# Performance work log

Hardware: AMD Instinct MI355X
Metric: run time of the kernel (lower is better)

The kernel has to match this reference:

```python
import jax, jax.numpy as jnp
import numpy as np

B, C, IMG, P = 16, 3, 224, 16
HP = IMG // P          # 14
NP = HP * HP           # 196 patches
PD = C * P * P         # 768 patch_dim
DIM, OUT = 768, 1024
DI, NS, DC, DTR = 2 * DIM, 16, 4, 48  # mamba: d_inner, d_state, d_conv, dt_rank
NL = 2


def _ln(x, g, b, eps=1e-5):
    m = x.mean(-1, keepdims=True)
    v = ((x - m) ** 2).mean(-1, keepdims=True)
    return (x - m) / jnp.sqrt(v + eps) * g + b


def _gelu(x):
    return jax.nn.gelu(x, approximate=False)


def _mamba_block(x, in_w, in_b, conv_w, conv_b, xproj_w, dt_w, dt_b, Alog, D, out_w, out_b):
    # x: [B, L, DIM]
    Bb, L, _ = x.shape
    xr = x @ in_w + in_b                      # [B, L, 2*DI]
    xi, res = jnp.split(xr, 2, axis=-1)
    # causal depthwise conv1d over L
    xp = jnp.pad(xi, ((0, 0), (DC - 1, 0), (0, 0)))
    xc = conv_b + sum(xp[:, k:k + L, :] * conv_w[:, k] for k in range(DC))
    xi = jax.nn.silu(xc)
    dbc = xi @ xproj_w                        # [B, L, DTR + 2*NS]
    delta = jax.nn.softplus(dbc[..., :DTR] @ dt_w + dt_b)   # [B, L, DI]
    Bm = dbc[..., DTR:DTR + NS]               # [B, L, NS]
    Cm = dbc[..., DTR + NS:]                  # [B, L, NS]
    A = -jnp.exp(Alog)                        # [DI, NS]
    dA = jnp.exp(delta[..., None] * A)                       # [B, L, DI, NS]
    dBu = delta[..., None] * Bm[:, :, None, :] * xi[..., None]

    def step(h, inp):
        dA_t, dBu_t, C_t = inp
        h = dA_t * h + dBu_t                  # [B, DI, NS]
        y = jnp.einsum('bdn,bn->bd', h, C_t)
        return h, y

    h0 = jnp.zeros((Bb, DI, NS), x.dtype)
    _, ys = jax.lax.scan(step, h0, (dA.transpose(1, 0, 2, 3),
                                    dBu.transpose(1, 0, 2, 3),
                                    Cm.transpose(1, 0, 2)))
    y = ys.transpose(1, 0, 2) + D * xi        # [B, L, DI]
    y = y * jax.nn.silu(res)
    return y @ out_w + out_b


def setup_inputs() -> dict:
    key = jax.random.key(0)
    ks = iter(jax.random.split(key, 40))

    def rn(shape, s=0.02):
        return jax.random.normal(next(ks), shape, jnp.float32) * s

    inp = {
        'img': jax.random.normal(next(ks), (B, C, IMG, IMG), jnp.float32),
        'sa_w': rn((1, 2, 7, 7), 0.1),
        'pe_w': rn((PD, DIM)), 'pe_b': jnp.zeros((DIM,), jnp.float32),
        'pos_emb': rn((1, NP, DIM), 1.0),
        'm_in_w': rn((NL, DIM, 2 * DI)), 'm_in_b': jnp.zeros((NL, 2 * DI), jnp.float32),
        'm_conv_w': rn((NL, DI, DC), 0.1), 'm_conv_b': jnp.zeros((NL, DI), jnp.float32),
        'm_xproj_w': rn((NL, DI, DTR + 2 * NS)),
        'm_dt_w': rn((NL, DTR, DI)), 'm_dt_b': rn((NL, DI), 0.01),
        'm_Alog': jnp.tile(jnp.log(jnp.arange(1, NS + 1, dtype=jnp.float32))[None, None, :], (NL, DI, 1)),
        'm_D': jnp.ones((NL, DI), jnp.float32),
        'm_out_w': rn((NL, DI, DIM)), 'm_out_b': jnp.zeros((NL, DIM), jnp.float32),
        'em_w': rn((DIM, OUT)), 'em_b': jnp.zeros((OUT,), jnp.float32),
        'em_g': jnp.ones((OUT,), jnp.float32), 'em_bt': jnp.zeros((OUT,), jnp.float32),
        'att_w': rn((OUT, OUT)), 'att_b': jnp.zeros((OUT,), jnp.float32),
        'att_g': jnp.ones((OUT,), jnp.float32), 'att_bt': jnp.zeros((OUT,), jnp.float32),
        'lat_g': jnp.ones((OUT,), jnp.float32), 'lat_bt': jnp.zeros((OUT,), jnp.float32),
    }
    return inp


def reference(img, sa_w, pe_w, pe_b, pos_emb,
              m_in_w, m_in_b, m_conv_w, m_conv_b, m_xproj_w,
              m_dt_w, m_dt_b, m_Alog, m_D, m_out_w, m_out_b,
              em_w, em_b, em_g, em_bt, att_w, att_b, att_g, att_bt,
              lat_g, lat_bt):
    # spatial attention gate
    avg = img.mean(axis=1, keepdims=True)
    mx = img.max(axis=1, keepdims=True)
    a = jnp.concatenate([avg, mx], axis=1)                    # [B,2,H,W]
    a = jax.lax.conv_general_dilated(a, sa_w, (1, 1), [(3, 3), (3, 3)],
                                     dimension_numbers=('NCHW', 'OIHW', 'NCHW'))
    img = img * jax.nn.sigmoid(a)
    # patchify: b c (h p1)(w p2) -> b (h w) (p1 p2 c)
    x = img.reshape(B, C, HP, P, HP, P).transpose(0, 2, 4, 3, 5, 1).reshape(B, NP, PD)
    x = x @ pe_w + pe_b                                       # [B, NP, DIM]
    x = x + pos_emb[:, :NP]
    for i in range(NL):
        x = _mamba_block(x, m_in_w[i], m_in_b[i], m_conv_w[i], m_conv_b[i],
                         m_xproj_w[i], m_dt_w[i], m_dt_b[i], m_Alog[i], m_D[i],
                         m_out_w[i], m_out_b[i])
    y = _gelu(_ln(x @ em_w + em_b, em_g, em_bt))              # [B, NP, OUT]
    z = jax.nn.softmax(_gelu(_ln(y @ att_w + att_b, att_g, att_bt)), axis=1)
    pooled = (y * z).sum(axis=1)                              # [B, OUT]
    return _ln(pooled, lat_g, lat_bt)
```

## Files before the change

### kernel.cpp

```cpp
#include <hip/hip_runtime.h>
#include <math.h>

static constexpr int NB = 16;
static constexpr int NC = 3;
static constexpr int IM = 224;
static constexpr int IMP = IM * IM;
static constexpr int HPq = 14;
static constexpr int NPq = 196;
static constexpr int OUTq = 1024;
static constexpr int DIq = 1536;
static constexpr int ROWS = NB * NPq;
static constexpr int MPAD = 3200;

typedef __bf16 bf8_t __attribute__((ext_vector_type(8)));
typedef float f4_t __attribute__((ext_vector_type(4)));
typedef const __attribute__((address_space(1))) unsigned int cgu32;
typedef __attribute__((address_space(3))) unsigned int lu32;

__device__ inline unsigned short f2bf(float x) {
    unsigned u = __builtin_bit_cast(unsigned, x);
    unsigned r = (u + 0x7FFFu + ((u >> 16) & 1u)) >> 16;
    return (unsigned short)r;
}
__device__ inline float bf2f(unsigned short v) {
    return __builtin_bit_cast(float, (unsigned)v << 16);
}
__device__ inline float fast_sig(float x) {
    return __builtin_amdgcn_rcpf(1.f + __expf(-x));
}

template<int CTRL>
__device__ inline float dpp_add(float x) {
    int v = __builtin_amdgcn_update_dpp(0, __builtin_bit_cast(int, x), CTRL, 0xF, 0xF, true);
    return x + __builtin_bit_cast(float, v);
}

__global__ __launch_bounds__(256) void k_avgmax(const float* __restrict__ img, float* __restrict__ am) {
    int idx = blockIdx.x * 256 + threadIdx.x;
    if (idx >= NB * IMP / 4) return;
    int p4 = (idx % (IMP / 4)) * 4, b = idx / (IMP / 4);
    const float* ib = img + (size_t)b * NC * IMP + p4;
    float4 c0 = *(const float4*)ib;
    float4 c1 = *(const float4*)(ib + IMP);
    float4 c2 = *(const float4*)(ib + 2 * IMP);
    float4 av, mx;
    av.x = (c0.x + c1.x + c2.x) * (1.f / 3.f); mx.x = fmaxf(c0.x, fmaxf(c1.x, c2.x));
    av.y = (c0.y + c1.y + c2.y) * (1.f / 3.f); mx.y = fmaxf(c0.y, fmaxf(c1.y, c2.y));
    av.z = (c0.z + c1.z + c2.z) * (1.f / 3.f); mx.z = fmaxf(c0.z, fmaxf(c1.z, c2.z));
    av.w = (c0.w + c1.w + c2.w) * (1.f / 3.f); mx.w = fmaxf(c0.w, fmaxf(c1.w, c2.w));
    *(float4*)(am + (size_t)(b * 2 + 0) * IMP + p4) = av;
    *(float4*)(am + (size_t)(b * 2 + 1) * IMP + p4) = mx;
}

__global__ __launch_bounds__(256) void k_gatepatch(const float* __restrict__ img, const float* __restrict__ am,
                                                   const float* __restrict__ saw, unsigned short* __restrict__ G) {
    int quad = blockIdx.x * 256 + threadIdx.x;
    if (quad >= NB * IMP / 4) return;
    int pq = quad % (IMP / 4), b = quad / (IMP / 4);
    int x0 = (pq % 56) * 4;
    int y = pq / 56;
    float acc0 = 0.f, acc1 = 0.f, acc2 = 0.f, acc3 = 0.f;
    const bool lok = (x0 >= 4), rok = (x0 <= IM - 8);
    #pragma unroll
    for (int ci = 0; ci < 2; ci++) {
        const float* amc = am + (size_t)(b * 2 + ci) * IMP;
        const float* wc = saw + ci * 49;
        #pragma unroll
        for (int kh = 0; kh < 7; kh++) {
            int yy = y + kh - 3;
            if (yy < 0 || yy >= IM) continue;
            const float* rowp = amc + yy * IM;
            float4 lv = lok ? *(const float4*)(rowp + x0 - 4) : make_float4(0.f, 0.f, 0.f, 0.f);
            float4 mv = *(const float4*)(rowp + x0);
            float4 rv = rok ? *(const float4*)(rowp + x0 + 4) : make_float4(0.f, 0.f, 0.f, 0.f);
            float f[12] = {lv.x, lv.y, lv.z, lv.w, mv.x, mv.y, mv.z, mv.w, rv.x, rv.y, rv.z, rv.w};
            #pragma unroll
            for (int kw = 0; kw < 7; kw++) {
                float w = wc[kh * 7 + kw];
                acc0 = fmaf(w, f[kw + 1], acc0);
                acc1 = fmaf(w, f[kw + 2], acc1);
                acc2 = fmaf(w, f[kw + 3], acc2);
                acc3 = fmaf(w, f[kw + 4], acc3);
            }
        }
    }
    float s0 = fast_sig(acc0), s1 = fast_sig(acc1), s2 = fast_sig(acc2), s3 = fast_sig(acc3);
    const float* ib = img + (size_t)b * NC * IMP + y * IM + x0;
    float4 c0 = *(const float4*)ib;
    float4 c1 = *(const float4*)(ib + IMP);
    float4 c2 = *(const float4*)(ib + 2 * IMP);
    int hy = y >> 4, py = y & 15, hx = x0 >> 4, px0 = x0 & 15;
    size_t base = ((size_t)(b * NPq + hy * HPq + hx) * 768) + (size_t)(py * 16 + px0) * 3;
    ushort4 o0, o1, o2;
    o0.x = f2bf(c0.x * s0); o0.y = f2bf(c1.x * s0); o0.z = f2bf(c2.x * s0);
    o0.w = f2bf(c0.y * s1);
    o1.x = f2bf(c1.y * s1); o1.y = f2bf(c2.y * s1);
    o1.z = f2bf(c0.z * s2); o1.w = f2bf(c1.z * s2);
    o2.x = f2bf(c2.z * s2);
    o2.y = f2bf(c0.w * s3); o2.z = f2bf(c1.w * s3); o2.w = f2bf(c2.w * s3);
    *(ushort4*)(G + base + 0) = o0;
    *(ushort4*)(G + base + 4) = o1;
    *(ushort4*)(G + base + 8) = o2;
}

__global__ __launch_bounds__(256) void k_transpose_bf(const float* __restrict__ W, unsigned short* __restrict__ Wt,
                                                      int K, int N) {
    __shared__ float t[32][33];
    int n0 = blockIdx.x * 32, k0 = blockIdx.y * 32;
    int c = threadIdx.x & 31, r8 = threadIdx.x >> 5;
    #pragma unroll
    for (int i = 0; i < 4; i++) {
        int r = r8 + i * 8;
        t[r][c] = W[(size_t)(k0 + r) * N + n0 + c];
    }
    __syncthreads();
    #pragma unroll
    for (int i = 0; i < 4; i++) {
        int r = r8 + i * 8;
        Wt[(size_t)(n0 + r) * K + k0 + c] = f2bf(t[c][r]);
    }
}

enum { EPI_NONE = 0, EPI_POSEMB = 1, EPI_SPLIT = 2 };

template<int EPI, bool CBF>
__global__ __launch_bounds__(256) void k_gemm_bf(const unsigned short* __restrict__ A,
                                                 const unsigned short* __restrict__ Wt,
                                                 const float* __restrict__ bias,
                                                 void* __restrict__ Cv, int ldc,
                                                 int M, int N, int K,
                                                 const float* __restrict__ extra,
                                                 float* __restrict__ C2) {
    constexpr int BM = 128, BN = 64;
    __shared__ __align__(16) unsigned short As[2][BM * 64];
    __shared__ __align__(16) unsigned short Bs[2][BN * 64];
    const int bm = blockIdx.y * BM, bn = blockIdx.x * BN;
    const int tid = threadIdx.x;
    const int lane = tid & 63;
    const int wbase = tid & ~63;
    const int wr = ((tid >> 7) & 1) * 64;
    const int wc = ((tid >> 6) & 1) * 32;
    const int lr = lane & 15, lq = lane >> 4;

    f4_t acc[4][2] = {};

    auto stage = [&](int buf, int k0) {
        #pragma unroll
        for (int i = 0; i < 4; i++) {
            int gid2 = i * 256 + tid;
            int r = gid2 >> 3, g = gid2 & 7;
            const unsigned short* src = A + (size_t)(bm + r) * K + k0 + ((g ^ (r & 7)) * 8);
            __builtin_amdgcn_global_load_lds((cgu32*)src,
                (lu32*)&As[buf][(i * 256 + wbase) * 8], 16, 0, 0);
        }
        #pragma unroll
        for (int i = 0; i < 2; i++) {
            int gid2 = i * 256 + tid;
            int r = gid2 >> 3, g = gid2 & 7;
            const unsigned short* src = Wt + (size_t)(bn + r) * K + k0 + ((g ^ (r & 7)) * 8);
            __builtin_amdgcn_global_load_lds((cgu32*)src,
                (lu32*)&Bs[buf][(i * 256 + wbase) * 8], 16, 0, 0);
        }
    };

    stage(0, 0);
    __syncthreads();
    int cur = 0;
    for (int k0 = 0; k0 < K; k0 += 64) {
        if (k0 + 64 < K) stage(cur ^ 1, k0 + 64);
        #pragma unroll
        for (int h = 0; h < 2; h++) {
            bf8_t af[4], bfr[2];
            #pragma unroll
            for (int mb = 0; mb < 4; mb++) {
                int row = wr + mb * 16 + lr;
                int g = h * 4 + lq;
                af[mb] = *(const bf8_t*)&As[cur][row * 64 + ((g ^ (row & 7)) * 8)];
            }
            #pragma unroll
            for (int nb = 0; nb < 2; nb++) {
                int rn = wc + nb * 16 + lr;
                int g = h * 4 + lq;
                bfr[nb] = *(const bf8_t*)&Bs[cur][rn * 64 + ((g ^ (rn & 7)) * 8)];
            }
            #pragma unroll
            for (int mb = 0; mb < 4; mb++)
                #pragma unroll
                for (int nb = 0; nb < 2; nb++)
                    acc[mb][nb] = __builtin_amdgcn_mfma_f32_16x16x32_bf16(af[mb], bfr[nb], acc[mb][nb], 0, 0, 0);
        }
        __syncthreads();
        cur ^= 1;
    }

    #pragma unroll
    for (int mb = 0; mb < 4; mb++) {
        #pragma unroll
        for (int nb = 0; nb < 2; nb++) {
            int col = bn + wc + nb * 16 + lr;
            #pragma unroll
            for (int q = 0; q < 4; q++) {
                int row = bm + wr + mb * 16 + lq * 4 + q;
                if (row < M) {
                    float v = acc[mb][nb][q];
                    if (bias) v += bias[col];
                    if (EPI == EPI_SPLIT) {
                        if (col < DIq) ((unsigned short*)Cv)[(size_t)row * DIq + col] = f2bf(v);
                        else           C2[(size_t)row * DIq + (col - DIq)] = v * fast_sig(v);
                    } else {
                        if (EPI == EPI_POSEMB) v += extra[(size_t)(row % NPq) * N + col];
                        if (CBF) ((unsigned short*)Cv)[(size_t)row * ldc + col] = f2bf(v);
                        else     ((float*)Cv)[(size_t)row * ldc + col] = v;
                    }
                }
            }
        }
    }
}

static constexpr int XP_KS = 4;
static constexpr int XP_KC = 1536 / XP_KS;

__global__ __launch_bounds__(256) void k_xproj_part(const float* __restrict__ xi2, const float* __restrict__ W,
                                                    float* __restrict__ part) {
    __shared__ float As[32][65];
    __shared__ __align__(16) float Bs[64][80];
    int m0 = blockIdx.x * 32;
    int kc0 = blockIdx.y * XP_KC;
    int tid = threadIdx.x;
    int row = tid >> 3, cg = (tid & 7) * 10;
    float acc[10] = {};
    for (int k0 = 0; k0 < XP_KC; k0 += 64) {
        #pragma unroll
        for (int i = 0; i < 2; i++) {
            int id = tid + i * 256;
            int r = id >> 4, c4 = (id & 15) * 4;
            float4 v = *(const float4*)(xi2 + (size_t)(m0 + r) * 1536 + kc0 + k0 + c4);
            As[r][c4] = v.x; As[r][c4 + 1] = v.y; As[r][c4 + 2] = v.z; As[r][c4 + 3] = v.w;
        }
        #pragma unroll
        for (int i = 0; i < 5; i++) {
            int id = tid + i * 256;
            int r = id / 20, c4 = (id % 20) * 4;
            *(float4*)&Bs[r][c4] = *(const float4*)(W + (size_t)(kc0 + k0 + r) * 80 + c4);
        }
        __syncthreads();
        #pragma unroll
        for (int kk = 0; kk < 64; kk++) {
            float a = As[row][kk];
            #pragma unroll
            for (int j = 0; j < 10; j++)
                acc[j] = fmaf(a, Bs[kk][cg + j], acc[j]);
        }
        __syncthreads();
    }
    float* p = part + ((size_t)blockIdx.y * ROWS + m0 + row) * 80 + cg;
    #pragma unroll
    for (int j = 0; j < 10; j++) p[j] = acc[j];
}

static constexpr int DT_RPB = 4;
__global__ __launch_bounds__(384) void k_dtred(const float* __restrict__ part, const float* __restrict__ W,
                                               const float* __restrict__ bias, float* __restrict__ de,
                                               float* __restrict__ dbc) {
    int r0 = blockIdx.x * DT_RPB;
    int tid = threadIdx.x;
    __shared__ float ds[DT_RPB][80];
    if (tid < DT_RPB * 80) {
        int row = tid / 80, col = tid % 80;
        const int S = ROWS * 80;
        const float* p = part + (size_t)(r0 + row) * 80 + col;
        float s = p[0] + p[S] + p[2 * S] + p[3 * S];
        ds[row][col] = s;
        if (col >= 48) dbc[(size_t)(r0 + row) * 80 + col] = s;
    }
    __syncthreads();
    int j = tid * 4;
    float4 b = *(const float4*)(bias + j);
    float4 a0 = b, a1 = b, a2 = b, a3 = b;
    for (int k = 0; k < 48; k++) {
        float4 w = *(const float4*)(W + (size_t)k * 1536 + j);
        float d0 = ds[0][k], d1 = ds[1][k], d2 = ds[2][k], d3 = ds[3][k];
        a0.x = fmaf(d0, w.x, a0.x); a0.y = fmaf(d0, w.y, a0.y); a0.z = fmaf(d0, w.z, a0.z); a0.w = fmaf(d0, w.w, a0.w);
        a1.x = fmaf(d1, w.x, a1.x); a1.y = fmaf(d1, w.y, a1.y); a1.z = fmaf(d1, w.z, a1.z); a1.w = fmaf(d1, w.w, a1.w);
        a2.x = fmaf(d2, w.x, a2.x); a2.y = fmaf(d2, w.y, a2.y); a2.z = fmaf(d2, w.z, a2.z); a2.w = fmaf(d2, w.w, a2.w);
        a3.x = fmaf(d3, w.x, a3.x); a3.y = fmaf(d3, w.y, a3.y); a3.z = fmaf(d3, w.z, a3.z); a3.w = fmaf(d3, w.w, a3.w);
    }
    auto sp = [](float v) { return (v > 20.f) ? v : log1pf(expf(v)); };
    float4 o;
    o.x = sp(a0.x); o.y = sp(a0.y); o.z = sp(a0.z); o.w = sp(a0.w);
    *(float4*)(de + (size_t)(r0 + 0) * 1536 + j) = o;
    o.x = sp(a1.x); o.y = sp(a1.y); o.z = sp(a1.z); o.w = sp(a1.w);
    *(float4*)(de + (size_t)(r0 + 1) * 1536 + j) = o;
    o.x = sp(a2.x); o.y = sp(a2.y); o.z = sp(a2.z); o.w = sp(a2.w);
    *(float4*)(de + (size_t)(r0 + 2) * 1536 + j) = o;
    o.x = sp(a3.x); o.y = sp(a3.y); o.z = sp(a3.z); o.w = sp(a3.w);
    *(float4*)(de + (size_t)(r0 + 3) * 1536 + j) = o;
}

__global__ __launch_bounds__(256) void k_conv_silu(const unsigned short* __restrict__ xr2, const float* __restrict__ cw,
                                                   const float* __restrict__ cb, float* __restrict__ xi2) {
    int idx4 = blockIdx.x * 256 + threadIdx.x;
    if (idx4 >= ROWS * DIq / 4) return;
    int d4 = (idx4 % (DIq / 4)) * 4;
    int bt = idx4 / (DIq / 4);
    int t = bt % NPq, b = bt / NPq;
    const unsigned short* base = xr2 + (size_t)b * NPq * DIq + d4;
    float4 s = *(const float4*)(cb + d4);
    float4 w0 = *(const float4*)(cw + (d4 + 0) * 4);
    float4 w1 = *(const float4*)(cw + (d4 + 1) * 4);
    float4 w2 = *(const float4*)(cw + (d4 + 2) * 4);
    float4 w3 = *(const float4*)(cw + (d4 + 3) * 4);
    if (t >= 3) {
        ushort4 v = *(const ushort4*)(base + (size_t)(t - 3) * DIq);
        s.x = fmaf(bf2f(v.x), w0.x, s.x); s.y = fmaf(bf2f(v.y), w1.x, s.y);
        s.z = fmaf(bf2f(v.z), w2.x, s.z); s.w = fmaf(bf2f(v.w), w3.x, s.w);
    }
    if (t >= 2) {
        ushort4 v = *(const ushort4*)(base + (size_t)(t - 2) * DIq);
        s.x = fmaf(bf2f(v.x), w0.y, s.x); s.y = fmaf(bf2f(v.y), w1.y, s.y);
        s.z = fmaf(bf2f(v.z), w2.y, s.z); s.w = fmaf(bf2f(v.w), w3.y, s.w);
    }
    if (t >= 1) {
        ushort4 v = *(const ushort4*)(base + (size_t)(t - 1) * DIq);
        s.x = fmaf(bf2f(v.x), w0.z, s.x); s.y = fmaf(bf2f(v.y), w1.z, s.y);
        s.z = fmaf(bf2f(v.z), w2.z, s.z); s.w = fmaf(bf2f(v.w), w3.z, s.w);
    }
    {
        ushort4 v = *(const ushort4*)(base + (size_t)t * DIq);
        s.x = fmaf(bf2f(v.x), w0.w, s.x); s.y = fmaf(bf2f(v.y), w1.w, s.y);
        s.z = fmaf(bf2f(v.z), w2.w, s.z); s.w = fmaf(bf2f(v.w), w3.w, s.w);
    }
    float4 xo;
    xo.x = s.x * fast_sig(s.x); xo.y = s.y * fast_sig(s.y);
    xo.z = s.z * fast_sig(s.z); xo.w = s.w * fast_sig(s.w);
    *(float4*)(xi2 + (size_t)bt * DIq + d4) = xo;
}

static constexpr int STB = 28;

__global__ __launch_bounds__(256) void k_scan(const float* __restrict__ delta, const float* __restrict__ xi2,
                                              const float* __restrict__ dbc, const float* __restrict__ sres,
                                              const float* __restrict__ Alog, const float* __restrict__ Dv,
                                              unsigned short* __restrict__ ys) {
    const int b = blockIdx.x;
    const int d0 = blockIdx.y * 32;
    const int tid = threadIdx.x;
    const int dl = tid >> 3;
    const int np = tid & 7;
    const int d = d0 + dl;
    const float A0 = -__expf(Alog[d * 16 + np]);
    const float A1 = -__expf(Alog[d * 16 + np + 8]);
    const float Dd = Dv[d];
    const int tr = tid >> 5;
    const int dls = tid & 31;

    __shared__ float4 sdu[2][STB][32];
    __shared__ float sbc[2][STB][32];

    const float* gde = delta + ((size_t)b * NPq + tr) * DIq + d0 + dls;
    const float* gu  = xi2   + ((size_t)b * NPq + tr) * DIq + d0 + dls;
    const float* gsr = sres  + ((size_t)b * NPq + tr) * DIq + d0 + dls;
    const float* gbc = dbc   + ((size_t)b * NPq + tr) * 80 + 48 + dls;
    unsigned short* gy = ys + (size_t)b * NPq * DIq + d;

    float rde[4], ru[4], rsr[4], rbc[4];

    auto stageLoad = [&](int c) {
        const int t0 = c * STB;
        #pragma unroll
        for (int j = 0; j < 3; j++) {
            int off = (t0 + 8 * j) * DIq;
            rde[j] = gde[off];
            ru[j]  = gu[off];
            rsr[j] = gsr[off];
            rbc[j] = gbc[(t0 + 8 * j) * 80];
        }
        if (tid < 128) {
            int off = (t0 + 24) * DIq;
            rde[3] = gde[off];
            ru[3]  = gu[off];
            rsr[3] = gsr[off];
            rbc[3] = gbc[(t0 + 24) * 80];
        }
    };
    auto stageWrite = [&](int buf) {
        const int pi = (dls & 7) * 4 + (dls >> 3);
        #pragma unroll
        for (int j = 0; j < 3; j++) {
            int t = tr + 8 * j;
            sdu[buf][t][dls] = make_float4(rde[j], ru[j], rsr[j], 0.f);
            sbc[buf][t][pi] = rbc[j];
        }
        if (tid < 128) {
            int t = tr + 24;
            sdu[buf][t][dls] = make_float4(rde[3], ru[3], rsr[3], 0.f);
            sbc[buf][t][pi] = rbc[3];
        }
    };

    stageLoad(0);
    stageWrite(0);
    __syncthreads();

    float h0 = 0.f, h1 = 0.f;
    int cur = 0;
    for (int c = 0; c < 7; c++) {
        if (c < 6) stageLoad(c + 1);
        #pragma unroll 4
        for (int t = 0; t < STB; t++) {
            float4 du = sdu[cur][t][dl];
            float4 bc = *(const float4*)&sbc[cur][t][np * 4];
            float a0 = __expf(du.x * A0), a1 = __expf(du.x * A1);
            float deu = du.x * du.y;
            h0 = fmaf(a0, h0, deu * bc.x);
            h1 = fmaf(a1, h1, deu * bc.y);
            float p = fmaf(h1, bc.w, h0 * bc.z);
            p = dpp_add<0xB1>(p);
            p = dpp_add<0x4E>(p);
            p = dpp_add<0x141>(p);
            if (np == 0) gy[(size_t)(c * STB + t) * DIq] = f2bf(fmaf(Dd, du.y, p) * du.z);
        }
        if (c < 6) stageWrite(cur ^ 1);
        __syncthreads();
        cur ^= 1;
    }
}

template<bool OBF>
__global__ __launch_bounds__(256) void k_ln_gelu(const float* __restrict__ in, const float* __restrict__ g,
                                                 const float* __restrict__ bt, void* __restrict__ outv) {
    int row = blockIdx.x;
    const float* x = in + (size_t)row * OUTq;
    float4 v = ((const float4*)x)[threadIdx.x];
    float s = v.x + v.y + v.z + v.w;
    float ss = v.x * v.x + v.y * v.y + v.z * v.z + v.w * v.w;
    #pragma unroll
    for (int off = 32; off >= 1; off >>= 1) { s += __shfl_down(s, off); ss += __shfl_down(ss, off); }
    __shared__ float sh[10];
    int wid = threadIdx.x >> 6, lid = threadIdx.x & 63;
    if (lid == 0) { sh[wid] = s; sh[4 + wid] = ss; }
    __syncthreads();
    if (threadIdx.x == 0) {
        float S = sh[0] + sh[1] + sh[2] + sh[3], SS = sh[4] + sh[5] + sh[6] + sh[7];
        float m = S * (1.f / OUTq);
        float var = SS * (1.f / OUTq) - m * m;
        sh[8] = m; sh[9] = rsqrtf(var + 1e-5f);
    }
    __syncthreads();
    float m = sh[8], rst = sh[9];
    float4 gv = ((const float4*)g)[threadIdx.x];
    float4 bv = ((const float4*)bt)[threadIdx.x];
    float4 o;
    float y0 = (v.x - m) * rst * gv.x + bv.x; o.x = 0.5f * y0 * (1.f + erff(y0 * 0.70710678118f));
    float y1 = (v.y - m) * rst * gv.y + bv.y; o.y = 0.5f * y1 * (1.f + erff(y1 * 0.70710678118f));
    float y2 = (v.z - m) * rst * gv.z + bv.z; o.z = 0.5f * y2 * (1.f + erff(y2 * 0.70710678118f));
    float y3 = (v.w - m) * rst * gv.w + bv.w; o.w = 0.5f * y3 * (1.f + erff(y3 * 0.70710678118f));
    if (OBF) {
        ushort4 o4;
        o4.x = f2bf(o.x); o4.y = f2bf(o.y); o4.z = f2bf(o.z); o4.w = f2bf(o.w);
        ((ushort4*)((unsigned short*)outv + (size_t)row * OUTq))[threadIdx.x] = o4;
    } else {
        ((float4*)((float*)outv + (size_t)row * OUTq))[threadIdx.x] = o;
    }
}

__global__ __launch_bounds__(256) void k_softpool(const float* __restrict__ gm, const unsigned short* __restrict__ ym,
                                                  float* __restrict__ pooled) {
    int b = blockIdx.y;
    int jl = threadIdx.x & 63;
    int j = blockIdx.x * 64 + jl;
    int tc = threadIdx.x >> 6;
    const float* gb = gm + (size_t)b * NPq * OUTq + j;
    const unsigned short* yb = ym + (size_t)b * NPq * OUTq + j;
    int t0 = tc * 49;
    float m = -1e30f, s = 0.f, ps = 0.f;
    for (int t = t0; t < t0 + 49; t++) {
        float g = gb[(size_t)t * OUTq];
        float y = bf2f(yb[(size_t)t * OUTq]);
        float mn = fmaxf(m, g);
        float sc = __expf(m - mn);
        float e = __expf(g - mn);
        s = fmaf(s, sc, e);
        ps = fmaf(ps, sc, y * e);
        m = mn;
    }
    __shared__ float sm[4][64], ssum[4][64], sps[4][64];
    sm[tc][jl] = m; ssum[tc][jl] = s; sps[tc][jl] = ps;
    __syncthreads();
    if (tc == 0) {
        float m0 = sm[0][jl], m1 = sm[1][jl], m2 = sm[2][jl], m3 = sm[3][jl];
        float mt = fmaxf(fmaxf(m0, m1), fmaxf(m2, m3));
        float e0 = __expf(m0 - mt), e1 = __expf(m1 - mt);
        float e2 = __expf(m2 - mt), e3 = __expf(m3 - mt);
        float st = ssum[0][jl] * e0 + ssum[1][jl] * e1 + ssum[2][jl] * e2 + ssum[3][jl] * e3;
        float pt = sps[0][jl] * e0 + sps[1][jl] * e1 + sps[2][jl] * e2 + sps[3][jl] * e3;
        pooled[b * OUTq + j] = pt / st;
    }
}

__global__ __launch_bounds__(256) void k_final_ln(const float* __restrict__ p, const float* __restrict__ g,
                                                  const float* __restrict__ bt, float* __restrict__ out) {
    int row = blockIdx.x;
    const float* x = p + (size_t)row * OUTq;
    float4 v = ((const float4*)x)[threadIdx.x];
    float s = v.x + v.y + v.z + v.w;
    float ss = v.x * v.x + v.y * v.y + v.z * v.z + v.w * v.w;
    #pragma unroll
    for (int off = 32; off >= 1; off >>= 1) { s += __shfl_down(s, off); ss += __shfl_down(ss, off); }
    __shared__ float sh[10];
    int wid = threadIdx.x >> 6, lid = threadIdx.x & 63;
    if (lid == 0) { sh[wid] = s; sh[4 + wid] = ss; }
    __syncthreads();
    if (threadIdx.x == 0) {
        float S = sh[0] + sh[1] + sh[2] + sh[3], SS = sh[4] + sh[5] + sh[6] + sh[7];
        float m = S * (1.f / OUTq);
        float var = SS * (1.f / OUTq) - m * m;
        sh[8] = m; sh[9] = rsqrtf(var + 1e-5f);
    }
    __syncthreads();
    float m = sh[8], rst = sh[9];
    float4 gv = ((const float4*)g)[threadIdx.x];
    float4 bv = ((const float4*)bt)[threadIdx.x];
    float4 o;
    o.x = (v.x - m) * rst * gv.x + bv.x;
    o.y = (v.y - m) * rst * gv.y + bv.y;
    o.z = (v.z - m) * rst * gv.z + bv.z;
    o.w = (v.w - m) * rst * gv.w + bv.w;
    ((float4*)(out + (size_t)row * OUTq))[threadIdx.x] = o;
}

extern "C" void kernel_launch(void* const* d_in, const int* in_sizes, int n_in,
                              void* d_out, int out_size, void* d_ws, size_t ws_size,
                              hipStream_t stream) {
    const float* img   = (const float*)d_in[0];
    const float* sa_w  = (const float*)d_in[1];
    const float* pe_w  = (const float*)d_in[2];
    const float* pe_b  = (const float*)d_in[3];
    const float* pos   = (const float*)d_in[4];
    const float* in_w  = (const float*)d_in[5];
    const float* in_b  = (const float*)d_in[6];
    const float* cv_w  = (const float*)d_in[7];
    const float* cv_b  = (const float*)d_in[8];
    const float* xp_w  = (const float*)d_in[9];
    const float* dt_w  = (const float*)d_in[10];
    const float* dt_b  = (const float*)d_in[11];
    const float* Alog  = (const float*)d_in[12];
    const float* Dv    = (const float*)d_in[13];
    const float* ot_w  = (const float*)d_in[14];
    const float* ot_b  = (const float*)d_in[15];
    const float* em_w  = (const float*)d_in[16];
    const float* em_b  = (const float*)d_in[17];
    const float* em_g  = (const float*)d_in[18];
    const float* em_bt = (const float*)d_in[19];
    const float* at_w  = (const float*)d_in[20];
    const float* at_b  = (const float*)d_in[21];
    const float* at_g  = (const float*)d_in[22];
    const float* at_bt = (const float*)d_in[23];
    const float* la_g  = (const float*)d_in[24];
    const float* la_bt = (const float*)d_in[25];

    char* ws = (char*)d_ws;
    auto al = [](size_t x) { return (x + 255) & ~(size_t)255; };
    size_t SZ_am   = (size_t)NB * 2 * IMP * 4;
    size_t SZ_G    = (size_t)MPAD * 768 * 2;
    size_t SZ_x    = (size_t)MPAD * 768 * 2;
    size_t SZ_xr2  = (size_t)ROWS * DIq * 2;
    size_t SZ_xi2  = (size_t)ROWS * DIq * 4;
    size_t SZ_de   = SZ_xi2;
    size_t SZ_dbc  = (size_t)ROWS * 80 * 4;
    size_t SZ_ys   = (size_t)MPAD * DIq * 2;
    size_t SZ_sres = SZ_xi2;
    size_t SZ_yem  = (size_t)MPAD * 1024 * 2;
    size_t SZ_pool = (size_t)NB * OUTq * 4;
    size_t SZ_part = (size_t)XP_KS * ROWS * 80 * 4;

    size_t o_am   = 0;
    size_t o_G    = al(o_am + SZ_am);
    size_t o_x    = al(o_G + SZ_G);
    size_t o_xr2  = al(o_x + SZ_x);
    size_t o_xi2  = al(o_xr2 + SZ_xr2);
    size_t o_de   = al(o_xi2 + SZ_xi2);
    size_t o_dbc  = al(o_de + SZ_de);
    size_t o_ys   = al(o_dbc + SZ_dbc);
    size_t o_sres = al(o_ys + SZ_ys);
    size_t o_yem  = al(o_sres + SZ_sres);
    size_t o_pool = al(o_yem + SZ_yem);
    size_t o_part = al(o_pool + SZ_pool);

    size_t o_wpe  = al(o_part + SZ_part);
    size_t o_win0 = al(o_wpe  + (size_t)768 * 768 * 2);
    size_t o_win1 = al(o_win0 + (size_t)3072 * 768 * 2);
    size_t o_wot0 = al(o_win1 + (size_t)3072 * 768 * 2);
    size_t o_wot1 = al(o_wot0 + (size_t)768 * 1536 * 2);
    size_t o_wem  = al(o_wot1 + (size_t)768 * 1536 * 2);
    size_t o_wat  = al(o_wem  + (size_t)1024 * 768 * 2);

    float* am    = (float*)(ws + o_am);
    unsigned short* G   = (unsigned short*)(ws + o_G);
    unsigned short* x   = (unsigned short*)(ws + o_x);
    unsigned short* xr2 = (unsigned short*)(ws + o_xr2);
    float* xi2   = (float*)(ws + o_xi2);
    float* de    = (float*)(ws + o_de);
    float* dbc   = (float*)(ws + o_dbc);
    unsigned short* ys = (unsigned short*)(ws + o_ys);
    float* sres  = (float*)(ws + o_sres);
    unsigned short* yem = (unsigned short*)(ws + o_yem);
    float* pool  = (float*)(ws + o_pool);
    float* part  = (float*)(ws + o_part);
    unsigned short* wpe  = (unsigned short*)(ws + o_wpe);
    unsigned short* win0 = (unsigned short*)(ws + o_win0);
    unsigned short* win1 = (unsigned short*)(ws + o_win1);
    unsigned short* wot0 = (unsigned short*)(ws + o_wot0);
    unsigned short* wot1 = (unsigned short*)(ws + o_wot1);
    unsigned short* wem  = (unsigned short*)(ws + o_wem);
    unsigned short* wat  = (unsigned short*)(ws + o_wat);
    float* t1  = (float*)(ws + o_de);
    float* t2  = (float*)(ws + o_xi2);
    float* gat = (float*)(ws + o_sres);

    k_transpose_bf<<<dim3(768 / 32, 768 / 32), 256, 0, stream>>>(pe_w, wpe, 768, 768);
    k_transpose_bf<<<dim3(3072 / 32, 768 / 32), 256, 0, stream>>>(in_w, win0, 768, 3072);
    k_transpose_bf<<<dim3(3072 / 32, 768 / 32), 256, 0, stream>>>(in_w + (size_t)768 * 3072, win1, 768, 3072);
    k_transpose_bf<<<dim3(768 / 32, 1536 / 32), 256, 0, stream>>>(ot_w, wot0, 1536, 768);
    k_transpose_bf<<<dim3(768 / 32, 1536 / 32), 256, 0, stream>>>(ot_w + (size_t)1536 * 768, wot1, 1536, 768);
    k_transpose_bf<<<dim3(1024 / 32, 768 / 32), 256, 0, stream>>>(em_w, wem, 768, 1024);
    k_transpose_bf<<<dim3(1024 / 32, 1024 / 32), 256, 0, stream>>>(at_w, wat, 1024, 1024);

    int nq = NB * IMP / 4;
    k_avgmax<<<(nq + 255) / 256, 256, 0, stream>>>(img, am);
    k_gatepatch<<<(nq + 255) / 256, 256, 0, stream>>>(img, am, sa_w, G);

    dim3 blk(256);
    k_gemm_bf<EPI_POSEMB, true><<<dim3(12, 25), blk, 0, stream>>>(G, wpe, pe_b, x, 768, ROWS, 768, 768,
                                                                  pos, nullptr);

    for (int l = 0; l < 2; l++) {
        const unsigned short* win = l ? win1 : win0;
        const unsigned short* wot = l ? wot1 : wot0;
        k_gemm_bf<EPI_SPLIT, true><<<dim3(48, 25), blk, 0, stream>>>(x, win, in_b + l * 3072, xr2, DIq,
                                                                     ROWS, 3072, 768, nullptr, sres);
        int nc4 = ROWS * DIq / 4;
        k_conv_silu<<<(nc4 + 255) / 256, 256, 0, stream>>>(xr2, cv_w + (size_t)l * DIq * 4, cv_b + l * DIq, xi2);
        k_xproj_part<<<dim3(ROWS / 32, XP_KS), blk, 0, stream>>>(xi2, xp_w + (size_t)l * 1536 * 80, part);
        k_dtred<<<ROWS / DT_RPB, 384, 0, stream>>>(part, dt_w + (size_t)l * 48 * 1536, dt_b + l * 1536, de, dbc);
        k_scan<<<dim3(16, 48), blk, 0, stream>>>(de, xi2, dbc, sres, Alog + (size_t)l * 1536 * 16,
                                                 Dv + l * 1536, ys);
        k_gemm_bf<EPI_NONE, true><<<dim3(12, 25), blk, 0, stream>>>(ys, wot, ot_b + l * 768, x, 768,
                                                                    ROWS, 768, 1536, nullptr, nullptr);
    }

    k_gemm_bf<EPI_NONE, false><<<dim3(16, 25), blk, 0, stream>>>(x, wem, em_b, t1, 1024, ROWS, 1024, 768,
                                                                 nullptr, nullptr);
    k_ln_gelu<true><<<ROWS, 256, 0, stream>>>(t1, em_g, em_bt, yem);
    k_gemm_bf<EPI_NONE, false><<<dim3(16, 25), blk, 0, stream>>>(yem, wat, at_b, t2, 1024, ROWS, 1024, 1024,
                                                                 nullptr, nullptr);
    k_ln_gelu<false><<<ROWS, 256, 0, stream>>>(t2, at_g, at_bt, gat);
    k_softpool<<<dim3(16, NB), 256, 0, stream>>>(gat, yem, pool);
    k_final_ln<<<NB, 256, 0, stream>>>(pool, la_g, la_bt, (float*)d_out);
}
```

Baseline: 503.7 us.

## Store mamba intermediates in bf16, merge transposes, add 128x128 in-proj GEMM

Moves xi2 (conv+silu output) and the silu(res) gate from fp32 to bf16 storage. The scan now packs both into one 32-bit word in shared memory, and the x-proj kernel reads bf16. The seven weight-transpose launches become a single kernel, and the in-projection uses a new 128x128-tile single-buffered GEMM. The intent is to cut memory traffic and launch overhead, at the cost of lower intermediate precision and no double buffering in the new GEMM.

```diff
diff --git a/kernel.cpp b/kernel.cpp
--- a/kernel.cpp
+++ b/kernel.cpp
@@ -14,6 +14,7 @@
 
 typedef __bf16 bf8_t __attribute__((ext_vector_type(8)));
 typedef float f4_t __attribute__((ext_vector_type(4)));
+typedef unsigned short us8 __attribute__((ext_vector_type(8)));
 typedef const __attribute__((address_space(1))) unsigned int cgu32;
 typedef __attribute__((address_space(3))) unsigned int lu32;
 
@@ -103,10 +104,23 @@
     *(ushort4*)(G + base + 8) = o2;
 }
 
-__global__ __launch_bounds__(256) void k_transpose_bf(const float* __restrict__ W, unsigned short* __restrict__ Wt,
-                                                      int K, int N) {
+__global__ __launch_bounds__(256) void k_transpose_all(const float* pe_w, const float* in_w, const float* ot_w,
+                                                       const float* em_w, const float* at_w,
+                                                       unsigned short* wpe, unsigned short* win0, unsigned short* win1,
+                                                       unsigned short* wot0, unsigned short* wot1,
+                                                       unsigned short* wem, unsigned short* wat) {
+    int bid = blockIdx.x;
+    const float* W; unsigned short* Wt; int K, N, local;
+    if (bid < 576)       { W = pe_w; Wt = wpe; K = 768; N = 768; local = bid; }
+    else if (bid < 2880) { W = in_w; Wt = win0; K = 768; N = 3072; local = bid - 576; }
+    else if (bid < 5184) { W = in_w + (size_t)768 * 3072; Wt = win1; K = 768; N = 3072; local = bid - 2880; }
+    else if (bid < 6336) { W = ot_w; Wt = wot0; K = 1536; N = 768; local = bid - 5184; }
+    else if (bid < 7488) { W = ot_w + (size_t)1536 * 768; Wt = wot1; K = 1536; N = 768; local = bid - 6336; }
+    else if (bid < 8256) { W = em_w; Wt = wem; K = 768; N = 1024; local = bid - 7488; }
+    else                 { W = at_w; Wt = wat; K = 1024; N = 1024; local = bid - 8256; }
+    int gx = N / 32;
+    int n0 = (local % gx) * 32, k0 = (local / gx) * 32;
     __shared__ float t[32][33];
-    int n0 = blockIdx.x * 32, k0 = blockIdx.y * 32;
     int c = threadIdx.x & 31, r8 = threadIdx.x >> 5;
     #pragma unroll
     for (int i = 0; i < 4; i++) {
@@ -121,7 +135,7 @@
     }
 }
 
-enum { EPI_NONE = 0, EPI_POSEMB = 1, EPI_SPLIT = 2 };
+enum { EPI_NONE = 0, EPI_POSEMB = 1 };
 
 template<int EPI, bool CBF>
 __global__ __launch_bounds__(256) void k_gemm_bf(const unsigned short* __restrict__ A,
@@ -129,8 +143,7 @@
                                                  const float* __restrict__ bias,
                                                  void* __restrict__ Cv, int ldc,
                                                  int M, int N, int K,
-                                                 const float* __restrict__ extra,
-                                                 float* __restrict__ C2) {
+                                                 const float* __restrict__ extra) {
     constexpr int BM = 128, BN = 64;
     __shared__ __align__(16) unsigned short As[2][BM * 64];
     __shared__ __align__(16) unsigned short Bs[2][BN * 64];
@@ -204,24 +217,96 @@
                 if (row < M) {
                     float v = acc[mb][nb][q];
                     if (bias) v += bias[col];
-                    if (EPI == EPI_SPLIT) {
-                        if (col < DIq) ((unsigned short*)Cv)[(size_t)row * DIq + col] = f2bf(v);
-                        else           C2[(size_t)row * DIq + (col - DIq)] = v * fast_sig(v);
-                    } else {
-                        if (EPI == EPI_POSEMB) v += extra[(size_t)(row % NPq) * N + col];
-                        if (CBF) ((unsigned short*)Cv)[(size_t)row * ldc + col] = f2bf(v);
-                        else     ((float*)Cv)[(size_t)row * ldc + col] = v;
-                    }
+                    if (EPI == EPI_POSEMB) v += extra[(size_t)(row % NPq) * N + col];
+                    if (CBF) ((unsigned short*)Cv)[(size_t)row * ldc + col] = f2bf(v);
+                    else     ((float*)Cv)[(size_t)row * ldc + col] = v;
                 }
             }
         }
     }
 }
 
+__global__ __launch_bounds__(256) void k_gemm_bf2(const unsigned short* __restrict__ A,
+                                                  const unsigned short* __restrict__ Wt,
+                                                  const float* __restrict__ bias,
+                                                  unsigned short* __restrict__ xr2,
+                                                  unsigned short* __restrict__ sres,
+                                                  int M, int K) {
+    constexpr int BM = 128;
+    __shared__ __align__(16) unsigned short As[BM * 64];
+    __shared__ __align__(16) unsigned short Bs[BM * 64];
+    const int bm = blockIdx.y * BM, bn = blockIdx.x * BM;
+    const int tid = threadIdx.x;
+    const int lane = tid & 63;
+    const int wbase = tid & ~63;
+    const int wid = tid >> 6;
+    const int wr = (wid >> 1) * 64;
+    const int wc = (wid & 1) * 64;
+    const int lr = lane & 15, lq = lane >> 4;
+
+    f4_t acc[4][4] = {};
+
+    for (int k0 = 0; k0 < K; k0 += 64) {
+        #pragma unroll
+        for (int i = 0; i < 4; i++) {
+            int gid2 = i * 256 + tid;
+            int r = gid2 >> 3, g = gid2 & 7;
+            const unsigned short* srcA = A + (size_t)(bm + r) * K + k0 + ((g ^ (r & 7)) * 8);
+            __builtin_amdgcn_global_load_lds((cgu32*)srcA,
+                (lu32*)&As[(i * 256 + wbase) * 8], 16, 0, 0);
+            const unsigned short* srcB = Wt + (size_t)(bn + r) * K + k0 + ((g ^ (r & 7)) * 8);
+            __builtin_amdgcn_global_load_lds((cgu32*)srcB,
+                (lu32*)&Bs[(i * 256 + wbase) * 8], 16, 0, 0);
+        }
+        __syncthreads();
+        #pragma unroll
+        for (int h = 0; h < 2; h++) {
+            bf8_t af[4], bfr[4];
+            #pragma unroll
+            for (int mb = 0; mb < 4; mb++) {
+                int row = wr + mb * 16 + lr;
+                int g = h * 4 + lq;
+                af[mb] = *(const bf8_t*)&As[row * 64 + ((g ^ (row & 7)) * 8)];
+            }
+            #pragma unroll
+            for (int nb = 0; nb < 4; nb++) {
+                int rn = wc + nb * 16 + lr;
+                int g = h * 4 + lq;
+                bfr[nb] = *(const bf8_t*)&Bs[rn * 64 + ((g ^ (rn & 7)) * 8)];
+            }
+            #pragma unroll
+            for (int mb = 0; mb < 4; mb++)
+                #pragma unroll
+                for (int nb = 0; nb < 4; nb++)
+                    acc[mb][nb] = __builtin_amdgcn_mfma_f32_16x16x32_bf16(af[mb], bfr[nb], acc[mb][nb], 0, 0, 0);
+        }
+        __syncthreads();
+    }
+
+    #pragma unroll
+    for (int mb = 0; mb < 4; mb++) {
+        #pragma unroll
+        for (int nb = 0; nb < 4; nb++) {
+            int col = bn + wc + nb * 16 + lr;
+            float bv = bias[col];
+            #pragma unroll
+            for (int q = 0; q < 4; q++) {
+                int row = bm + wr + mb * 16 + lq * 4 + q;
+                if (row < M) {
+                    float v = acc[mb][nb][q] + bv;
+                    if (col < DIq) xr2[(size_t)row * DIq + col] = f2bf(v);
+                    else           sres[(size_t)row * DIq + (col - DIq)] = f2bf(v * fast_sig(v));
+                }
+            }
+        }
+    }
+}
+
 static constexpr int XP_KS = 4;
 static constexpr int XP_KC = 1536 / XP_KS;
 
-__global__ __launch_bounds__(256) void k_xproj_part(const float* __restrict__ xi2, const float* __restrict__ W,
+__global__ __launch_bounds__(256) void k_xproj_part(const unsigned short* __restrict__ xi2b,
+                                                    const float* __restrict__ W,
                                                     float* __restrict__ part) {
     __shared__ float As[32][65];
     __shared__ __align__(16) float Bs[64][80];
@@ -231,12 +316,11 @@
     int row = tid >> 3, cg = (tid & 7) * 10;
     float acc[10] = {};
     for (int k0 = 0; k0 < XP_KC; k0 += 64) {
-        #pragma unroll
-        for (int i = 0; i < 2; i++) {
-            int id = tid + i * 256;
-            int r = id >> 4, c4 = (id & 15) * 4;
-            float4 v = *(const float4*)(xi2 + (size_t)(m0 + r) * 1536 + kc0 + k0 + c4);
-            As[r][c4] = v.x; As[r][c4 + 1] = v.y; As[r][c4 + 2] = v.z; As[r][c4 + 3] = v.w;
+        {
+            int r = tid >> 3, c8 = (tid & 7) * 8;
+            us8 v = *(const us8*)(xi2b + (size_t)(m0 + r) * 1536 + kc0 + k0 + c8);
+            #pragma unroll
+            for (int j = 0; j < 8; j++) As[r][c8 + j] = bf2f(v[j]);
         }
         #pragma unroll
         for (int i = 0; i < 5; i++) {
@@ -299,7 +383,7 @@
 }
 
 __global__ __launch_bounds__(256) void k_conv_silu(const unsigned short* __restrict__ xr2, const float* __restrict__ cw,
-                                                   const float* __restrict__ cb, float* __restrict__ xi2) {
+                                                   const float* __restrict__ cb, unsigned short* __restrict__ xi2b) {
     int idx4 = blockIdx.x * 256 + threadIdx.x;
     if (idx4 >= ROWS * DIq / 4) return;
     int d4 = (idx4 % (DIq / 4)) * 4;
@@ -331,16 +415,16 @@
         s.x = fmaf(bf2f(v.x), w0.w, s.x); s.y = fmaf(bf2f(v.y), w1.w, s.y);
         s.z = fmaf(bf2f(v.z), w2.w, s.z); s.w = fmaf(bf2f(v.w), w3.w, s.w);
     }
-    float4 xo;
-    xo.x = s.x * fast_sig(s.x); xo.y = s.y * fast_sig(s.y);
-    xo.z = s.z * fast_sig(s.z); xo.w = s.w * fast_sig(s.w);
-    *(float4*)(xi2 + (size_t)bt * DIq + d4) = xo;
+    ushort4 xo;
+    xo.x = f2bf(s.x * fast_sig(s.x)); xo.y = f2bf(s.y * fast_sig(s.y));
+    xo.z = f2bf(s.z * fast_sig(s.z)); xo.w = f2bf(s.w * fast_sig(s.w));
+    *(ushort4*)(xi2b + (size_t)bt * DIq + d4) = xo;
 }
 
 static constexpr int STB = 28;
 
-__global__ __launch_bounds__(256) void k_scan(const float* __restrict__ delta, const float* __restrict__ xi2,
-                                              const float* __restrict__ dbc, const float* __restrict__ sres,
+__global__ __launch_bounds__(256) void k_scan(const float* __restrict__ delta, const unsigned short* __restrict__ xi2b,
+                                              const float* __restrict__ dbc, const unsigned short* __restrict__ sresb,
                                               const float* __restrict__ Alog, const float* __restrict__ Dv,
                                               unsigned short* __restrict__ ys) {
     const int b = blockIdx.x;
@@ -355,16 +439,17 @@
     const int tr = tid >> 5;
     const int dls = tid & 31;
 
-    __shared__ float4 sdu[2][STB][32];
+    __shared__ float2 sdu[2][STB][32];
     __shared__ float sbc[2][STB][32];
 
     const float* gde = delta + ((size_t)b * NPq + tr) * DIq + d0 + dls;
-    const float* gu  = xi2   + ((size_t)b * NPq + tr) * DIq + d0 + dls;
-    const float* gsr = sres  + ((size_t)b * NPq + tr) * DIq + d0 + dls;
-    const float* gbc = dbc   + ((size_t)b * NPq + tr) * 80 + 48 + dls;
+    const unsigned short* gu  = xi2b  + ((size_t)b * NPq + tr) * DIq + d0 + dls;
+    const unsigned short* gsr = sresb + ((size_t)b * NPq + tr) * DIq + d0 + dls;
+    const float* gbc = dbc + ((size_t)b * NPq + tr) * 80 + 48 + dls;
     unsigned short* gy = ys + (size_t)b * NPq * DIq + d;
 
-    float rde[4], ru[4], rsr[4], rbc[4];
+    float rde[4], rbc[4];
+    unsigned short ruu[4], rss[4];
 
     auto stageLoad = [&](int c) {
         const int t0 = c * STB;
@@ -372,15 +457,15 @@
         for (int j = 0; j < 3; j++) {
             int off = (t0 + 8 * j) * DIq;
             rde[j] = gde[off];
-            ru[j]  = gu[off];
-            rsr[j] = gsr[off];
+            ruu[j] = gu[off];
+            rss[j] = gsr[off];
             rbc[j] = gbc[(t0 + 8 * j) * 80];
         }
         if (tid < 128) {
             int off = (t0 + 24) * DIq;
             rde[3] = gde[off];
-            ru[3]  = gu[off];
-            rsr[3] = gsr[off];
+            ruu[3] = gu[off];
+            rss[3] = gsr[off];
             rbc[3] = gbc[(t0 + 24) * 80];
         }
     };
@@ -389,12 +474,14 @@
         #pragma unroll
         for (int j = 0; j < 3; j++) {
             int t = tr + 8 * j;
-            sdu[buf][t][dls] = make_float4(rde[j], ru[j], rsr[j], 0.f);
+            unsigned pk = ((unsigned)ruu[j] << 16) | rss[j];
+            sdu[buf][t][dls] = make_float2(rde[j], __builtin_bit_cast(float, pk));
             sbc[buf][t][pi] = rbc[j];
         }
         if (tid < 128) {
             int t = tr + 24;
-            sdu[buf][t][dls] = make_float4(rde[3], ru[3], rsr[3], 0.f);
+            unsigned pk = ((unsigned)ruu[3] << 16) | rss[3];
+            sdu[buf][t][dls] = make_float2(rde[3], __builtin_bit_cast(float, pk));
             sbc[buf][t][pi] = rbc[3];
         }
     };
@@ -409,17 +496,20 @@
         if (c < 6) stageLoad(c + 1);
         #pragma unroll 4
         for (int t = 0; t < STB; t++) {
-            float4 du = sdu[cur][t][dl];
+            float2 duv = sdu[cur][t][dl];
             float4 bc = *(const float4*)&sbc[cur][t][np * 4];
-            float a0 = __expf(du.x * A0), a1 = __expf(du.x * A1);
-            float deu = du.x * du.y;
+            unsigned bits = __builtin_bit_cast(unsigned, duv.y);
+            float u  = __builtin_bit_cast(float, bits & 0xFFFF0000u);
+            float sr = __builtin_bit_cast(float, bits << 16);
+            float a0 = __expf(duv.x * A0), a1 = __expf(duv.x * A1);
+            float deu = duv.x * u;
             h0 = fmaf(a0, h0, deu * bc.x);
             h1 = fmaf(a1, h1, deu * bc.y);
             float p = fmaf(h1, bc.w, h0 * bc.z);
             p = dpp_add<0xB1>(p);
             p = dpp_add<0x4E>(p);
             p = dpp_add<0x141>(p);
-            if (np == 0) gy[(size_t)(c * STB + t) * DIq] = f2bf(fmaf(Dd, du.y, p) * du.z);
+            if (np == 0) gy[(size_t)(c * STB + t) * DIq] = f2bf(fmaf(Dd, u, p) * sr);
         }
         if (c < 6) stageWrite(cur ^ 1);
         __syncthreads();
@@ -566,11 +656,11 @@
     size_t SZ_G    = (size_t)MPAD * 768 * 2;
     size_t SZ_x    = (size_t)MPAD * 768 * 2;
     size_t SZ_xr2  = (size_t)ROWS * DIq * 2;
-    size_t SZ_xi2  = (size_t)ROWS * DIq * 4;
-    size_t SZ_de   = SZ_xi2;
+    size_t SZ_xi2  = (size_t)ROWS * DIq * 2;
+    size_t SZ_de   = (size_t)ROWS * DIq * 4;
     size_t SZ_dbc  = (size_t)ROWS * 80 * 4;
     size_t SZ_ys   = (size_t)MPAD * DIq * 2;
-    size_t SZ_sres = SZ_xi2;
+    size_t SZ_sres = (size_t)ROWS * DIq * 2;
     size_t SZ_yem  = (size_t)MPAD * 1024 * 2;
     size_t SZ_pool = (size_t)NB * OUTq * 4;
     size_t SZ_part = (size_t)XP_KS * ROWS * 80 * 4;
@@ -600,11 +690,11 @@
     unsigned short* G   = (unsigned short*)(ws + o_G);
     unsigned short* x   = (unsigned short*)(ws + o_x);
     unsigned short* xr2 = (unsigned short*)(ws + o_xr2);
-    float* xi2   = (float*)(ws + o_xi2);
+    unsigned short* xi2b = (unsigned short*)(ws + o_xi2);
     float* de    = (float*)(ws + o_de);
     float* dbc   = (float*)(ws + o_dbc);
     unsigned short* ys = (unsigned short*)(ws + o_ys);
-    float* sres  = (float*)(ws + o_sres);
+    unsigned short* sresb = (unsigned short*)(ws + o_sres);
     unsigned short* yem = (unsigned short*)(ws + o_yem);
     float* pool  = (float*)(ws + o_pool);
     float* part  = (float*)(ws + o_part);
@@ -616,45 +706,36 @@
     unsigned short* wem  = (unsigned short*)(ws + o_wem);
     unsigned short* wat  = (unsigned short*)(ws + o_wat);
     float* t1  = (float*)(ws + o_de);
-    float* t2  = (float*)(ws + o_xi2);
-    float* gat = (float*)(ws + o_sres);
-
-    k_transpose_bf<<<dim3(768 / 32, 768 / 32), 256, 0, stream>>>(pe_w, wpe, 768, 768);
-    k_transpose_bf<<<dim3(3072 / 32, 768 / 32), 256, 0, stream>>>(in_w, win0, 768, 3072);
-    k_transpose_bf<<<dim3(3072 / 32, 768 / 32), 256, 0, stream>>>(in_w + (size_t)768 * 3072, win1, 768, 3072);
-    k_transpose_bf<<<dim3(768 / 32, 1536 / 32), 256, 0, stream>>>(ot_w, wot0, 1536, 768);
-    k_transpose_bf<<<dim3(768 / 32, 1536 / 32), 256, 0, stream>>>(ot_w + (size_t)1536 * 768, wot1, 1536, 768);
-    k_transpose_bf<<<dim3(1024 / 32, 768 / 32), 256, 0, stream>>>(em_w, wem, 768, 1024);
-    k_transpose_bf<<<dim3(1024 / 32, 1024 / 32), 256, 0, stream>>>(at_w, wat, 1024, 1024);
+    float* t2  = (float*)(ws + o_xr2);
+    float* gat = (float*)(ws + o_ys);
+
+    k_transpose_all<<<9280, 256, 0, stream>>>(pe_w, in_w, ot_w, em_w, at_w,
+                                              wpe, win0, win1, wot0, wot1, wem, wat);
 
     int nq = NB * IMP / 4;
     k_avgmax<<<(nq + 255) / 256, 256, 0, stream>>>(img, am);
     k_gatepatch<<<(nq + 255) / 256, 256, 0, stream>>>(img, am, sa_w, G);
 
     dim3 blk(256);
-    k_gemm_bf<EPI_POSEMB, true><<<dim3(12, 25), blk, 0, stream>>>(G, wpe, pe_b, x, 768, ROWS, 768, 768,
-                                                                  pos, nullptr);
+    k_gemm_bf<EPI_POSEMB, true><<<dim3(12, 25), blk, 0, stream>>>(G, wpe, pe_b, x, 768, ROWS, 768, 768, pos);
 
     for (int l = 0; l < 2; l++) {
         const unsigned short* win = l ? win1 : win0;
         const unsigned short* wot = l ? wot1 : wot0;
-        k_gemm_bf<EPI_SPLIT, true><<<dim3(48, 25), blk, 0, stream>>>(x, win, in_b + l * 3072, xr2, DIq,
-                                                                     ROWS, 3072, 768, nullptr, sres);
+        k_gemm_bf2<<<dim3(24, 25), blk, 0, stream>>>(x, win, in_b + l * 3072, xr2, sresb, ROWS, 768);
         int nc4 = ROWS * DIq / 4;
-        k_conv_silu<<<(nc4 + 255) / 256, 256, 0, stream>>>(xr2, cv_w + (size_t)l * DIq * 4, cv_b + l * DIq, xi2);
-        k_xproj_part<<<dim3(ROWS / 32, XP_KS), blk, 0, stream>>>(xi2, xp_w + (size_t)l * 1536 * 80, part);
+        k_conv_silu<<<(nc4 + 255) / 256, 256, 0, stream>>>(xr2, cv_w + (size_t)l * DIq * 4, cv_b + l * DIq, xi2b);
+        k_xproj_part<<<dim3(ROWS / 32, XP_KS), blk, 0, stream>>>(xi2b, xp_w + (size_t)l * 1536 * 80, part);
         k_dtred<<<ROWS / DT_RPB, 384, 0, stream>>>(part, dt_w + (size_t)l * 48 * 1536, dt_b + l * 1536, de, dbc);
-        k_scan<<<dim3(16, 48), blk, 0, stream>>>(de, xi2, dbc, sres, Alog + (size_t)l * 1536 * 16,
+        k_scan<<<dim3(16, 48), blk, 0, stream>>>(de, xi2b, dbc, sresb, Alog + (size_t)l * 1536 * 16,
                                                  Dv + l * 1536, ys);
         k_gemm_bf<EPI_NONE, true><<<dim3(12, 25), blk, 0, stream>>>(ys, wot, ot_b + l * 768, x, 768,
-                                                                    ROWS, 768, 1536, nullptr, nullptr);
-    }
-
-    k_gemm_bf<EPI_NONE, false><<<dim3(16, 25), blk, 0, stream>>>(x, wem, em_b, t1, 1024, ROWS, 1024, 768,
-                                                                 nullptr, nullptr);
+                                                                    ROWS, 768, 1536, nullptr);
+    }
+
+    k_gemm_bf<EPI_NONE, false><<<dim3(16, 25), blk, 0, stream>>>(x, wem, em_b, t1, 1024, ROWS, 1024, 768, nullptr);
     k_ln_gelu<true><<<ROWS, 256, 0, stream>>>(t1, em_g, em_bt, yem);
-    k_gemm_bf<EPI_NONE, false><<<dim3(16, 25), blk, 0, stream>>>(yem, wat, at_b, t2, 1024, ROWS, 1024, 1024,
-                                                                 nullptr, nullptr);
+    k_gemm_bf<EPI_NONE, false><<<dim3(16, 25), blk, 0, stream>>>(yem, wat, at_b, t2, 1024, ROWS, 1024, 1024, nullptr);
     k_ln_gelu<false><<<ROWS, 256, 0, stream>>>(t2, at_g, at_bt, gat);
     k_softpool<<<dim3(16, NB), 256, 0, stream>>>(gat, yem, pool);
     k_final_ln<<<NB, 256, 0, stream>>>(pool, la_g, la_bt, (float*)d_out);
```

After: 467.1 us. 7.3% less time.
